# Kernel tuning notes

Hardware: AMD Instinct MI355X
Metric: run time of the kernel (lower is better)

Reference implementation:

```python
import jax, jax.numpy as jnp
import numpy as np

N = 100000   # nodes
E = 3200000  # edges (avg degree 32)
F = 10       # input features
H = 20       # hidden dim
G = 512      # graphs in batch
L = 2        # labels


def xavier(key, shape):
    fan_in, fan_out = shape[0], shape[1]
    a = jnp.sqrt(6.0 / (fan_in + fan_out))
    return jax.random.uniform(key, shape, jnp.float32, -a, a)


def setup_inputs() -> dict:
    key = jax.random.key(0)
    ks = jax.random.split(key, 12)
    x = jax.random.normal(ks[0], (N, F), jnp.float32)
    edge_index = jax.random.randint(ks[1], (2, E), 0, N, jnp.int64)
    batch = jnp.sort(jax.random.randint(ks[2], (N,), 0, G, jnp.int64))
    return {
        "x": x,
        "edge_index": edge_index,
        "batch": batch,
        # layer 1: F -> H
        "W_rel1": xavier(ks[3], (F, H)), "b1": jnp.zeros((H,), jnp.float32),
        "W_root1": xavier(ks[4], (F, H)),
        # layer 2: H -> H
        "W_rel2": xavier(ks[5], (H, H)), "b2": jnp.zeros((H,), jnp.float32),
        "W_root2": xavier(ks[6], (H, H)),
        # layer 3: H -> H
        "W_rel3": xavier(ks[7], (H, H)), "b3": jnp.zeros((H,), jnp.float32),
        "W_root3": xavier(ks[8], (H, H)),
        # readout linear: 2H -> L
        "W_lin": xavier(ks[9], (2 * H, L)), "b_lin": jnp.zeros((L,), jnp.float32),
    }


def _graph_conv(x, src, dst, W_rel, b, W_root):
    # PyG GraphConv: out = lin_rel(sum_{j->i} x_j) + lin_root(x_i)
    agg = jax.ops.segment_sum(x[src], dst, num_segments=N)  # [N, d_in]
    return agg @ W_rel + b + x @ W_root


def reference(x, edge_index, batch, W_rel1, b1, W_root1, W_rel2, b2, W_root2,
              W_rel3, b3, W_root3, W_lin, b_lin):
    src, dst = edge_index[0], edge_index[1]
    h = jax.nn.relu(_graph_conv(x, src, dst, W_rel1, b1, W_root1))
    h = jax.nn.relu(_graph_conv(h, src, dst, W_rel2, b2, W_root2))
    h = jax.nn.relu(_graph_conv(h, src, dst, W_rel3, b3, W_root3))  # [N, H]
    # global max / mean pool over graphs
    maxp = jax.ops.segment_max(h, batch, num_segments=G)            # [G, H]
    sump = jax.ops.segment_sum(h, batch, num_segments=G)            # [G, H]
    counts = jax.ops.segment_sum(jnp.ones((h.shape[0], 1), h.dtype), batch,
                                 num_segments=G)                    # [G, 1]
    nonempty = counts > 0
    maxp = jnp.where(nonempty, maxp, 0.0)
    meanp = sump / jnp.maximum(counts, 1.0)
    pooled = jnp.concatenate([maxp, meanp], axis=-1)                # [G, 2H]
    return pooled @ W_lin + b_lin
```

## Files before the change

### kernel.cpp

```cpp
#include <hip/hip_runtime.h>
#include <hip/hip_bf16.h>

#define NN 100000
#define FF 10
#define HH 20
#define GG 512
#define LL 2

#define NB 500
#define BNODES 200
#define CAP 7168
#define HB 100
#define SCAP 3712
#define TILE 4096
#define SRC_BITS 17
#define SRC_MASK 0x1FFFFu

__device__ inline unsigned short f2bf(float f) {
  unsigned u = __float_as_uint(f);
  unsigned r = u + 0x7FFFu + ((u >> 16) & 1u);
  return (unsigned short)(r >> 16);
}
__device__ inline float bflo(unsigned u) { return __uint_as_float(u << 16); }
__device__ inline float bfhi(unsigned u) { return __uint_as_float(u & 0xFFFF0000u); }

__global__ __launch_bounds__(256) void cast_init_kernel(
    const float* __restrict__ x, unsigned short* __restrict__ xb,
    float* __restrict__ sump, int* __restrict__ maxp, float* __restrict__ cnt,
    int* __restrict__ cursor, int n) {
  int i = blockIdx.x * 256 + threadIdx.x;
  if (i < n) xb[i] = f2bf(__builtin_nontemporal_load(x + i));
  if (i < GG * HH) {
    sump[i] = 0.0f;
    maxp[i] = 0;
  }
  if (i < GG) cnt[i] = 0.0f;
  if (i < NB) cursor[i] = 0;
}

__global__ __launch_bounds__(512) void multisplit_kernel(
    const int* __restrict__ src, const int* __restrict__ dst,
    int* __restrict__ cursor, unsigned int* __restrict__ pay, int E) {
  __shared__ int lhist[NB];
  __shared__ int lofs[NB];
  __shared__ int gbase[NB];
  __shared__ int lcur[NB];
  __shared__ unsigned int sord[TILE];
  __shared__ unsigned short sdbk[TILE];
  __shared__ int ss[512];
  int t = threadIdx.x;
  if (t < NB) lhist[t] = 0;
  __syncthreads();

  int base = blockIdx.x * TILE;
  int count = E - base;
  if (count > TILE) count = TILE;

  for (int i = t; i < count; i += 512)
    atomicAdd(&lhist[dst[base + i] / BNODES], 1);
  __syncthreads();

  int own = (t < NB) ? lhist[t] : 0;
  ss[t] = own;
  __syncthreads();
  for (int off = 1; off < 512; off <<= 1) {
    int a0 = (t >= off) ? ss[t - off] : 0;
    __syncthreads();
    ss[t] += a0;
    __syncthreads();
  }
  if (t < NB) {
    lofs[t] = ss[t] - own;
    int bo = own ? atomicAdd(&cursor[t], own) : 0;
    if (bo > CAP - own) bo = CAP - own;
    gbase[t] = t * CAP + bo;
    lcur[t] = 0;
  }
  __syncthreads();

  for (int i = t; i < count; i += 512) {
    int e = base + i;
    int d = __builtin_nontemporal_load(dst + e);
    int s = __builtin_nontemporal_load(src + e);
    int bk = d / BNODES;
    int ld = d - bk * BNODES;
    int r = atomicAdd(&lcur[bk], 1);
    int slot = lofs[bk] + r;
    sord[slot] = ((unsigned)ld << SRC_BITS) | (unsigned)s;
    sdbk[slot] = (unsigned short)bk;
  }
  __syncthreads();

  for (int i = t; i < count; i += 512) {
    int bk = sdbk[i];
    pay[gbase[bk] + (i - lofs[bk])] = sord[i];
  }
}

__global__ __launch_bounds__(256) void bucket_csr_kernel(
    const unsigned int* __restrict__ pay, const int* __restrict__ cursor,
    int* __restrict__ srt, int* __restrict__ rofs, int* __restrict__ rend) {
  __shared__ int lhist[BNODES];
  __shared__ int lofs[BNODES];
  __shared__ int lcur[BNODES];
  __shared__ int ss[256];
  int b = blockIdx.x;
  int t = threadIdx.x;
  int k0 = b * CAP;
  int ecnt = cursor[b];
  if (ecnt > CAP) ecnt = CAP;

  if (t < BNODES) lhist[t] = 0;
  __syncthreads();
  for (int k = t; k < ecnt; k += 256)
    atomicAdd(&lhist[pay[k0 + k] >> SRC_BITS], 1);
  __syncthreads();

  int own = (t < BNODES) ? lhist[t] : 0;
  ss[t] = own;
  __syncthreads();
  for (int off = 1; off < 256; off <<= 1) {
    int a0 = (t >= off) ? ss[t - off] : 0;
    __syncthreads();
    ss[t] += a0;
    __syncthreads();
  }
  if (t < BNODES) {
    int ex = ss[t] - own;
    lofs[t] = ex;
    lcur[t] = 0;
    rofs[b * BNODES + t] = k0 + ex;
    rend[b * BNODES + t] = k0 + ex + own;
  }
  __syncthreads();

  for (int k = t; k < ecnt; k += 256) {
    unsigned p = pay[k0 + k];
    int ld = p >> SRC_BITS;
    int r = atomicAdd(&lcur[ld], 1);
    srt[k0 + lofs[ld] + r] = (int)(p & SRC_MASK);
  }
}

template<int DIN>
__global__ __launch_bounds__(512) void bucket_layer_kernel(
    const unsigned short* __restrict__ hin, const int* __restrict__ srt,
    const int* __restrict__ rofs, const int* __restrict__ rend,
    const float* __restrict__ Wrel, const float* __restrict__ bias,
    const float* __restrict__ Wroot, unsigned short* __restrict__ hout) {
  constexpr int AST = (DIN == 10) ? 11 : 21;
  constexpr int CH = DIN / 5;
  __shared__ int sSrc[SCAP];
  __shared__ float acc[HB * AST];
  __shared__ unsigned short roots[HB * DIN];
  __shared__ float sWrel[DIN * HH];
  __shared__ float sWroot[DIN * HH];
  __shared__ float sb[HH];
  __shared__ int sRofs[HB];
  __shared__ int sRend[HB];
  __shared__ int sSeg0, sSegLen;
  int b2 = blockIdx.x;
  int t = threadIdx.x;
  int nbase = b2 * HB;

  for (int i = t; i < DIN * HH; i += 512) {
    sWrel[i] = Wrel[i];
    sWroot[i] = Wroot[i];
  }
  if (t < HH) sb[t] = bias[t];
  if (t < HB) {
    sRofs[t] = rofs[nbase + t];
    sRend[t] = rend[nbase + t];
  }
  if (t == 0) {
    int s0 = rofs[nbase];
    int sl = rend[nbase + HB - 1] - s0;
    sSeg0 = s0;
    sSegLen = sl < SCAP ? sl : SCAP;
  }
  {
    const unsigned* rs = (const unsigned*)(hin + (size_t)nbase * DIN);
    unsigned* rd = (unsigned*)roots;
    for (int i = t; i < HB * DIN / 2; i += 512) rd[i] = rs[i];
  }
  __syncthreads();

  int seg0 = sSeg0, seglen = sSegLen;
  for (int i = t; i < seglen; i += 512) sSrc[i] = srt[seg0 + i];
  __syncthreads();

  if (t < HB * 5) {
    int ln = t / 5;
    int c = t - ln * 5;
    int k0 = sRofs[ln] - seg0;
    int k1 = sRend[ln] - seg0;
    if (k1 > seglen) k1 = seglen;
    float a0 = 0, a1 = 0, a2 = 0, a3 = 0;
    const unsigned short* xb = hin + c * CH;
    if (CH == 4) {
      for (int k = k0; k < k1; k++) {
        uint2 u = *(const uint2*)(xb + (size_t)sSrc[k] * DIN);
        a0 += bflo(u.x);
        a1 += bfhi(u.x);
        a2 += bflo(u.y);
        a3 += bfhi(u.y);
      }
    } else {
      for (int k = k0; k < k1; k++) {
        unsigned u = *(const unsigned*)(xb + (size_t)sSrc[k] * DIN);
        a0 += bflo(u);
        a1 += bfhi(u);
      }
    }
    float* a = acc + ln * AST + c * CH;
    if (CH == 4) {
      a[0] = a0; a[1] = a1; a[2] = a2; a[3] = a3;
    } else {
      a[0] = a0; a[1] = a1;
    }
  }
  __syncthreads();

  for (int idx = t; idx < HB * HH; idx += 512) {
    int ln = idx / HH;
    int j = idx - ln * HH;
    const float* a = acc + ln * AST;
    const unsigned short* r = roots + ln * DIN;
    float v = sb[j];
#pragma unroll
    for (int f = 0; f < DIN; f++) {
      v += a[f] * sWrel[f * HH + j];
      v += bflo((unsigned)r[f]) * sWroot[f * HH + j];
    }
    hout[(size_t)nbase * HH + idx] = f2bf(fmaxf(v, 0.0f));
  }
}

__global__ __launch_bounds__(512) void bucket_layer_pool_kernel(
    const unsigned short* __restrict__ hin, const int* __restrict__ srt,
    const int* __restrict__ rofs, const int* __restrict__ rend,
    const float* __restrict__ Wrel, const float* __restrict__ bias,
    const float* __restrict__ Wroot, const int* __restrict__ batch,
    float* __restrict__ sump, int* __restrict__ maxp,
    float* __restrict__ cnt) {
  constexpr int DIN = 20;
  constexpr int AST = 21;
  __shared__ int sSrc[SCAP];
  __shared__ float acc[HB * AST];
  __shared__ unsigned short roots[HB * DIN];
  __shared__ int sBatch[HB];
  __shared__ float sWrel[DIN * HH];
  __shared__ float sWroot[DIN * HH];
  __shared__ float sb[HH];
  __shared__ int sRofs[HB];
  __shared__ int sRend[HB];
  __shared__ int sSeg0, sSegLen;
  int b2 = blockIdx.x;
  int t = threadIdx.x;
  int nbase = b2 * HB;

  for (int i = t; i < DIN * HH; i += 512) {
    sWrel[i] = Wrel[i];
    sWroot[i] = Wroot[i];
  }
  if (t < HH) sb[t] = bias[t];
  if (t < HB) {
    sRofs[t] = rofs[nbase + t];
    sRend[t] = rend[nbase + t];
    sBatch[t] = batch[nbase + t];
  }
  if (t == 0) {
    int s0 = rofs[nbase];
    int sl = rend[nbase + HB - 1] - s0;
    sSeg0 = s0;
    sSegLen = sl < SCAP ? sl : SCAP;
  }
  {
    const unsigned* rs = (const unsigned*)(hin + (size_t)nbase * DIN);
    unsigned* rd = (unsigned*)roots;
    for (int i = t; i < HB * DIN / 2; i += 512) rd[i] = rs[i];
  }
  __syncthreads();

  int seg0 = sSeg0, seglen = sSegLen;
  for (int i = t; i < seglen; i += 512) sSrc[i] = srt[seg0 + i];
  __syncthreads();

  if (t < HB * 5) {
    int ln = t / 5;
    int c = t - ln * 5;
    int k0 = sRofs[ln] - seg0;
    int k1 = sRend[ln] - seg0;
    if (k1 > seglen) k1 = seglen;
    float a0 = 0, a1 = 0, a2 = 0, a3 = 0;
    const unsigned short* xb = hin + c * 4;
    for (int k = k0; k < k1; k++) {
      uint2 u = *(const uint2*)(xb + (size_t)sSrc[k] * 20);
      a0 += bflo(u.x);
      a1 += bfhi(u.x);
      a2 += bflo(u.y);
      a3 += bfhi(u.y);
    }
    float* a = acc + ln * AST + c * 4;
    a[0] = a0; a[1] = a1; a[2] = a2; a[3] = a3;
  }
  __syncthreads();

  float vreg[4];
#pragma unroll
  for (int u = 0; u < 4; u++) {
    int idx = t + u * 512;
    if (idx < HB * HH) {
      int ln = idx / HH;
      int j = idx - ln * HH;
      const float* a = acc + ln * AST;
      const unsigned short* r = roots + ln * DIN;
      float v = sb[j];
#pragma unroll
      for (int f = 0; f < DIN; f++) {
        v += a[f] * sWrel[f * HH + j];
        v += bflo((unsigned)r[f]) * sWroot[f * HH + j];
      }
      vreg[u] = fmaxf(v, 0.0f);
    }
  }
  __syncthreads();
#pragma unroll
  for (int u = 0; u < 4; u++) {
    int idx = t + u * 512;
    if (idx < HB * HH) {
      int ln = idx / HH;
      int j = idx - ln * HH;
      acc[ln * AST + j] = vreg[u];
    }
  }
  __syncthreads();

  int g0 = sBatch[0];
  int g1 = sBatch[HB - 1];
  int ngr = g1 - g0 + 1;
  for (int it = t; it < ngr * HH; it += 512) {
    int gi = it / HH;
    int j = it - gi * HH;
    int g = g0 + gi;
    float s = 0.0f, m = 0.0f;
    int c = 0;
    for (int ln = 0; ln < HB; ln++) {
      if (sBatch[ln] == g) {
        float v = acc[ln * AST + j];
        s += v;
        m = fmaxf(m, v);
        c++;
      }
    }
    if (c) {
      atomicAdd(&sump[g * HH + j], s);
      atomicMax(&maxp[g * HH + j], __float_as_int(m));
      if (j == 0) atomicAdd(&cnt[g], (float)c);
    }
  }
}

__global__ __launch_bounds__(256) void readout_kernel(
    const float* __restrict__ sump, const int* __restrict__ maxp,
    const float* __restrict__ cnt, const float* __restrict__ Wlin,
    const float* __restrict__ blin, float* __restrict__ out) {
  int idx = blockIdx.x * 256 + threadIdx.x;
  if (idx >= GG * LL) return;
  int g = idx / LL;
  int l = idx - g * LL;
  float c = cnt[g];
  float inv = 1.0f / fmaxf(c, 1.0f);
  float acc = blin[l];
#pragma unroll
  for (int j = 0; j < HH; j++) {
    float mx = __int_as_float(maxp[g * HH + j]);
    float mean = sump[g * HH + j] * inv;
    acc += mx * Wlin[j * LL + l];
    acc += mean * Wlin[(HH + j) * LL + l];
  }
  out[idx] = acc;
}

extern "C" void kernel_launch(void* const* d_in, const int* in_sizes, int n_in,
                              void* d_out, int out_size, void* d_ws,
                              size_t ws_size, hipStream_t stream) {
  const float* x = (const float*)d_in[0];
  const int* edge_index = (const int*)d_in[1];
  const int* batch = (const int*)d_in[2];
  const float* W_rel1 = (const float*)d_in[3];
  const float* b1 = (const float*)d_in[4];
  const float* W_root1 = (const float*)d_in[5];
  const float* W_rel2 = (const float*)d_in[6];
  const float* b2 = (const float*)d_in[7];
  const float* W_root2 = (const float*)d_in[8];
  const float* W_rel3 = (const float*)d_in[9];
  const float* b3 = (const float*)d_in[10];
  const float* W_root3 = (const float*)d_in[11];
  const float* W_lin = (const float*)d_in[12];
  const float* b_lin = (const float*)d_in[13];
  float* out = (float*)d_out;

  const int E = in_sizes[1] / 2;
  const int n_nodes = in_sizes[0] / FF;
  const int* src = edge_index;
  const int* dst = edge_index + E;

  unsigned int* pay = (unsigned int*)d_ws;
  int* srt = (int*)(pay + (size_t)NB * CAP);
  int* rofs = srt + (size_t)NB * CAP;
  int* rend = rofs + NN;
  int* cursor = rend + NN;
  float* sump = (float*)(cursor + 512);
  int* maxp = (int*)(sump + GG * HH);
  float* cnt = (float*)(maxp + GG * HH);
  unsigned short* xb = (unsigned short*)(cnt + 512);
  unsigned short* h1 = xb + (size_t)NN * FF;
  unsigned short* h2 = h1 + (size_t)NN * HH;

  const int edge_tiles = (E + TILE - 1) / TILE;

  cast_init_kernel<<<(n_nodes * FF + 255) / 256, 256, 0, stream>>>(
      x, xb, sump, maxp, cnt, cursor, n_nodes * FF);

  multisplit_kernel<<<edge_tiles, 512, 0, stream>>>(src, dst, cursor, pay, E);
  bucket_csr_kernel<<<NB, 256, 0, stream>>>(pay, cursor, srt, rofs, rend);

  bucket_layer_kernel<FF><<<NB * 2, 512, 0, stream>>>(
      xb, srt, rofs, rend, W_rel1, b1, W_root1, h1);
  bucket_layer_kernel<HH><<<NB * 2, 512, 0, stream>>>(
      h1, srt, rofs, rend, W_rel2, b2, W_root2, h2);
  bucket_layer_pool_kernel<<<NB * 2, 512, 0, stream>>>(
      h2, srt, rofs, rend, W_rel3, b3, W_root3, batch, sump, maxp, cnt);

  readout_kernel<<<(GG * LL + 255) / 256, 256, 0, stream>>>(
      sump, maxp, cnt, W_lin, b_lin, out);
}
```

Baseline: 259.1 us.

## Pad bf16 feature rows to 16/24 and balance edge gathers across threads

Feature buffers are stored padded (16 bf16 for input, 24 for hidden) so every gather can fetch 8 features with one 16-byte load. Edge work in each node block is now split into equal-length contiguous ranges per thread group, with a binary search to find the starting node and shared-memory atomics to combine partial sums at node boundaries. The previous scheme gave one thread per node and so suffered load imbalance. The dense transform is also vectorised with float4 weight reads and fp32 roots. The cost is extra bytes per gathered row for the padding and shared atomics where ranges cross nodes.

```diff
diff --git a/kernel.cpp b/kernel.cpp
--- a/kernel.cpp
+++ b/kernel.cpp
@@ -15,6 +15,8 @@
 #define TILE 4096
 #define SRC_BITS 17
 #define SRC_MASK 0x1FFFFu
+#define XPAD 16
+#define HPAD 24
 
 __device__ inline unsigned short f2bf(float f) {
   unsigned u = __float_as_uint(f);
@@ -27,9 +29,15 @@
 __global__ __launch_bounds__(256) void cast_init_kernel(
     const float* __restrict__ x, unsigned short* __restrict__ xb,
     float* __restrict__ sump, int* __restrict__ maxp, float* __restrict__ cnt,
-    int* __restrict__ cursor, int n) {
+    int* __restrict__ cursor, int n16) {
   int i = blockIdx.x * 256 + threadIdx.x;
-  if (i < n) xb[i] = f2bf(__builtin_nontemporal_load(x + i));
+  if (i < n16) {
+    int node = i >> 4;
+    int f = i & 15;
+    float v = 0.0f;
+    if (f < FF) v = __builtin_nontemporal_load(x + (size_t)node * FF + f);
+    xb[i] = f2bf(v);
+  }
   if (i < GG * HH) {
     sump[i] = 0.0f;
     maxp[i] = 0;
@@ -142,19 +150,20 @@
   }
 }
 
-template<int DIN>
-__global__ __launch_bounds__(512) void bucket_layer_kernel(
+template<int DL, int DSI, int DSO>
+__global__ __launch_bounds__(512) void layer_kernel(
     const unsigned short* __restrict__ hin, const int* __restrict__ srt,
     const int* __restrict__ rofs, const int* __restrict__ rend,
     const float* __restrict__ Wrel, const float* __restrict__ bias,
     const float* __restrict__ Wroot, unsigned short* __restrict__ hout) {
-  constexpr int AST = (DIN == 10) ? 11 : 21;
-  constexpr int CH = DIN / 5;
+  constexpr int CL = DSI / 8;
+  constexpr int NG = 512 / CL;
+  constexpr int AST = DSI + 1;
   __shared__ int sSrc[SCAP];
   __shared__ float acc[HB * AST];
-  __shared__ unsigned short roots[HB * DIN];
-  __shared__ float sWrel[DIN * HH];
-  __shared__ float sWroot[DIN * HH];
+  __shared__ float rootsf[HB * DL];
+  __shared__ __align__(16) float sWrel[DL * HH];
+  __shared__ __align__(16) float sWroot[DL * HH];
   __shared__ float sb[HH];
   __shared__ int sRofs[HB];
   __shared__ int sRend[HB];
@@ -163,7 +172,7 @@
   int t = threadIdx.x;
   int nbase = b2 * HB;
 
-  for (int i = t; i < DIN * HH; i += 512) {
+  for (int i = t; i < DL * HH; i += 512) {
     sWrel[i] = Wrel[i];
     sWroot[i] = Wroot[i];
   }
@@ -178,88 +187,116 @@
     sSeg0 = s0;
     sSegLen = sl < SCAP ? sl : SCAP;
   }
-  {
-    const unsigned* rs = (const unsigned*)(hin + (size_t)nbase * DIN);
-    unsigned* rd = (unsigned*)roots;
-    for (int i = t; i < HB * DIN / 2; i += 512) rd[i] = rs[i];
-  }
+  for (int i = t; i < HB * (DL / 2); i += 512) {
+    int ln = i / (DL / 2);
+    int p = i - ln * (DL / 2);
+    unsigned u = *(const unsigned*)(hin + (size_t)(nbase + ln) * DSI + 2 * p);
+    rootsf[ln * DL + 2 * p] = bflo(u);
+    rootsf[ln * DL + 2 * p + 1] = bfhi(u);
+  }
+  for (int i = t; i < HB * AST; i += 512) acc[i] = 0.0f;
   __syncthreads();
 
   int seg0 = sSeg0, seglen = sSegLen;
-  for (int i = t; i < seglen; i += 512) sSrc[i] = srt[seg0 + i];
+  for (int i = t; i < seglen; i += 512)
+    sSrc[i] = __builtin_nontemporal_load(srt + seg0 + i);
+  __syncthreads();
+
+  int g = t / CL;
+  int c = t - g * CL;
+  if (g < NG) {
+    int W = (seglen + NG - 1) / NG;
+    int a = g * W;
+    if (a > seglen) a = seglen;
+    int b = a + W;
+    if (b > seglen) b = seglen;
+    if (a < b) {
+      int lo = 0, hi = HB - 1;
+      while (lo < hi) {
+        int mid = (lo + hi + 1) >> 1;
+        if (sRofs[mid] - seg0 <= a) lo = mid; else hi = mid - 1;
+      }
+      int ln = lo;
+      const unsigned short* basep = hin + c * 8;
+      float a0 = 0, a1 = 0, a2 = 0, a3 = 0, a4 = 0, a5 = 0, a6 = 0, a7 = 0;
+      int k = a;
+      while (k < b) {
+        int lim = sRend[ln] - seg0;
+        if (lim > b) lim = b;
+#pragma clang loop unroll_count(4)
+        for (; k < lim; ++k) {
+          int s = sSrc[k];
+          uint4 u = *(const uint4*)(basep + (size_t)s * DSI);
+          a0 += bflo(u.x); a1 += bfhi(u.x);
+          a2 += bflo(u.y); a3 += bfhi(u.y);
+          a4 += bflo(u.z); a5 += bfhi(u.z);
+          a6 += bflo(u.w); a7 += bfhi(u.w);
+        }
+        float* ap = acc + ln * AST + c * 8;
+        atomicAdd(ap + 0, a0); atomicAdd(ap + 1, a1);
+        atomicAdd(ap + 2, a2); atomicAdd(ap + 3, a3);
+        atomicAdd(ap + 4, a4); atomicAdd(ap + 5, a5);
+        atomicAdd(ap + 6, a6); atomicAdd(ap + 7, a7);
+        a0 = a1 = a2 = a3 = a4 = a5 = a6 = a7 = 0.0f;
+        ln++;
+      }
+    }
+  }
   __syncthreads();
 
   if (t < HB * 5) {
     int ln = t / 5;
-    int c = t - ln * 5;
-    int k0 = sRofs[ln] - seg0;
-    int k1 = sRend[ln] - seg0;
-    if (k1 > seglen) k1 = seglen;
-    float a0 = 0, a1 = 0, a2 = 0, a3 = 0;
-    const unsigned short* xb = hin + c * CH;
-    if (CH == 4) {
-      for (int k = k0; k < k1; k++) {
-        uint2 u = *(const uint2*)(xb + (size_t)sSrc[k] * DIN);
-        a0 += bflo(u.x);
-        a1 += bfhi(u.x);
-        a2 += bflo(u.y);
-        a3 += bfhi(u.y);
-      }
-    } else {
-      for (int k = k0; k < k1; k++) {
-        unsigned u = *(const unsigned*)(xb + (size_t)sSrc[k] * DIN);
-        a0 += bflo(u);
-        a1 += bfhi(u);
-      }
+    int jg = t - ln * 5;
+    int j0 = jg * 4;
+    float v0 = sb[j0], v1 = sb[j0 + 1], v2 = sb[j0 + 2], v3 = sb[j0 + 3];
+    const float* ap = acc + ln * AST;
+    const float* rp = rootsf + ln * DL;
+#pragma unroll
+    for (int f = 0; f < DL; ++f) {
+      float af = ap[f], rf = rp[f];
+      float4 wr = *(const float4*)(sWrel + f * HH + j0);
+      float4 wo = *(const float4*)(sWroot + f * HH + j0);
+      v0 += af * wr.x + rf * wo.x;
+      v1 += af * wr.y + rf * wo.y;
+      v2 += af * wr.z + rf * wo.z;
+      v3 += af * wr.w + rf * wo.w;
     }
-    float* a = acc + ln * AST + c * CH;
-    if (CH == 4) {
-      a[0] = a0; a[1] = a1; a[2] = a2; a[3] = a3;
-    } else {
-      a[0] = a0; a[1] = a1;
-    }
-  }
-  __syncthreads();
-
-  for (int idx = t; idx < HB * HH; idx += 512) {
-    int ln = idx / HH;
-    int j = idx - ln * HH;
-    const float* a = acc + ln * AST;
-    const unsigned short* r = roots + ln * DIN;
-    float v = sb[j];
+    unsigned short* orow = hout + (size_t)(nbase + ln) * DSO;
+    uint2 o;
+    o.x = ((unsigned)f2bf(fmaxf(v1, 0.0f)) << 16) | f2bf(fmaxf(v0, 0.0f));
+    o.y = ((unsigned)f2bf(fmaxf(v3, 0.0f)) << 16) | f2bf(fmaxf(v2, 0.0f));
+    *(uint2*)(orow + j0) = o;
+  }
+  if (t < HB) {
+    unsigned short* orow = hout + (size_t)(nbase + t) * DSO;
 #pragma unroll
-    for (int f = 0; f < DIN; f++) {
-      v += a[f] * sWrel[f * HH + j];
-      v += bflo((unsigned)r[f]) * sWroot[f * HH + j];
-    }
-    hout[(size_t)nbase * HH + idx] = f2bf(fmaxf(v, 0.0f));
-  }
-}
-
-__global__ __launch_bounds__(512) void bucket_layer_pool_kernel(
+    for (int e = HH; e < DSO; ++e) orow[e] = 0;
+  }
+}
+
+__global__ __launch_bounds__(512) void layer_pool_kernel(
     const unsigned short* __restrict__ hin, const int* __restrict__ srt,
     const int* __restrict__ rofs, const int* __restrict__ rend,
     const float* __restrict__ Wrel, const float* __restrict__ bias,
     const float* __restrict__ Wroot, const int* __restrict__ batch,
     float* __restrict__ sump, int* __restrict__ maxp,
     float* __restrict__ cnt) {
-  constexpr int DIN = 20;
-  constexpr int AST = 21;
+  constexpr int DL = 20, DSI = 24, CL = 3, NG = 170, AST = 25;
   __shared__ int sSrc[SCAP];
   __shared__ float acc[HB * AST];
-  __shared__ unsigned short roots[HB * DIN];
-  __shared__ int sBatch[HB];
-  __shared__ float sWrel[DIN * HH];
-  __shared__ float sWroot[DIN * HH];
+  __shared__ float rootsf[HB * DL];
+  __shared__ __align__(16) float sWrel[DL * HH];
+  __shared__ __align__(16) float sWroot[DL * HH];
   __shared__ float sb[HH];
   __shared__ int sRofs[HB];
   __shared__ int sRend[HB];
+  __shared__ int sBatch[HB];
   __shared__ int sSeg0, sSegLen;
   int b2 = blockIdx.x;
   int t = threadIdx.x;
   int nbase = b2 * HB;
 
-  for (int i = t; i < DIN * HH; i += 512) {
+  for (int i = t; i < DL * HH; i += 512) {
     sWrel[i] = Wrel[i];
     sWroot[i] = Wroot[i];
   }
@@ -275,64 +312,89 @@
     sSeg0 = s0;
     sSegLen = sl < SCAP ? sl : SCAP;
   }
-  {
-    const unsigned* rs = (const unsigned*)(hin + (size_t)nbase * DIN);
-    unsigned* rd = (unsigned*)roots;
-    for (int i = t; i < HB * DIN / 2; i += 512) rd[i] = rs[i];
-  }
+  for (int i = t; i < HB * (DL / 2); i += 512) {
+    int ln = i / (DL / 2);
+    int p = i - ln * (DL / 2);
+    unsigned u = *(const unsigned*)(hin + (size_t)(nbase + ln) * DSI + 2 * p);
+    rootsf[ln * DL + 2 * p] = bflo(u);
+    rootsf[ln * DL + 2 * p + 1] = bfhi(u);
+  }
+  for (int i = t; i < HB * AST; i += 512) acc[i] = 0.0f;
   __syncthreads();
 
   int seg0 = sSeg0, seglen = sSegLen;
-  for (int i = t; i < seglen; i += 512) sSrc[i] = srt[seg0 + i];
-  __syncthreads();
-
+  for (int i = t; i < seglen; i += 512)
+    sSrc[i] = __builtin_nontemporal_load(srt + seg0 + i);
+  __syncthreads();
+
+  int g = t / CL;
+  int c = t - g * CL;
+  if (g < NG) {
+    int W = (seglen + NG - 1) / NG;
+    int a = g * W;
+    if (a > seglen) a = seglen;
+    int b = a + W;
+    if (b > seglen) b = seglen;
+    if (a < b) {
+      int lo = 0, hi = HB - 1;
+      while (lo < hi) {
+        int mid = (lo + hi + 1) >> 1;
+        if (sRofs[mid] - seg0 <= a) lo = mid; else hi = mid - 1;
+      }
+      int ln = lo;
+      const unsigned short* basep = hin + c * 8;
+      float a0 = 0, a1 = 0, a2 = 0, a3 = 0, a4 = 0, a5 = 0, a6 = 0, a7 = 0;
+      int k = a;
+      while (k < b) {
+        int lim = sRend[ln] - seg0;
+        if (lim > b) lim = b;
+#pragma clang loop unroll_count(4)
+        for (; k < lim; ++k) {
+          int s = sSrc[k];
+          uint4 u = *(const uint4*)(basep + (size_t)s * DSI);
+          a0 += bflo(u.x); a1 += bfhi(u.x);
+          a2 += bflo(u.y); a3 += bfhi(u.y);
+          a4 += bflo(u.z); a5 += bfhi(u.z);
+          a6 += bflo(u.w); a7 += bfhi(u.w);
+        }
+        float* ap = acc + ln * AST + c * 8;
+        atomicAdd(ap + 0, a0); atomicAdd(ap + 1, a1);
+        atomicAdd(ap + 2, a2); atomicAdd(ap + 3, a3);
+        atomicAdd(ap + 4, a4); atomicAdd(ap + 5, a5);
+        atomicAdd(ap + 6, a6); atomicAdd(ap + 7, a7);
+        a0 = a1 = a2 = a3 = a4 = a5 = a6 = a7 = 0.0f;
+        ln++;
+      }
+    }
+  }
+  __syncthreads();
+
+  float v0 = 0, v1 = 0, v2 = 0, v3 = 0;
+  int ln0 = 0, j0 = 0;
   if (t < HB * 5) {
-    int ln = t / 5;
-    int c = t - ln * 5;
-    int k0 = sRofs[ln] - seg0;
-    int k1 = sRend[ln] - seg0;
-    if (k1 > seglen) k1 = seglen;
-    float a0 = 0, a1 = 0, a2 = 0, a3 = 0;
-    const unsigned short* xb = hin + c * 4;
-    for (int k = k0; k < k1; k++) {
-      uint2 u = *(const uint2*)(xb + (size_t)sSrc[k] * 20);
-      a0 += bflo(u.x);
-      a1 += bfhi(u.x);
-      a2 += bflo(u.y);
-      a3 += bfhi(u.y);
+    ln0 = t / 5;
+    int jg = t - ln0 * 5;
+    j0 = jg * 4;
+    v0 = sb[j0]; v1 = sb[j0 + 1]; v2 = sb[j0 + 2]; v3 = sb[j0 + 3];
+    const float* ap = acc + ln0 * AST;
+    const float* rp = rootsf + ln0 * DL;
+#pragma unroll
+    for (int f = 0; f < DL; ++f) {
+      float af = ap[f], rf = rp[f];
+      float4 wr = *(const float4*)(sWrel + f * HH + j0);
+      float4 wo = *(const float4*)(sWroot + f * HH + j0);
+      v0 += af * wr.x + rf * wo.x;
+      v1 += af * wr.y + rf * wo.y;
+      v2 += af * wr.z + rf * wo.z;
+      v3 += af * wr.w + rf * wo.w;
     }
-    float* a = acc + ln * AST + c * 4;
-    a[0] = a0; a[1] = a1; a[2] = a2; a[3] = a3;
-  }
-  __syncthreads();
-
-  float vreg[4];
-#pragma unroll
-  for (int u = 0; u < 4; u++) {
-    int idx = t + u * 512;
-    if (idx < HB * HH) {
-      int ln = idx / HH;
-      int j = idx - ln * HH;
-      const float* a = acc + ln * AST;
-      const unsigned short* r = roots + ln * DIN;
-      float v = sb[j];
-#pragma unroll
-      for (int f = 0; f < DIN; f++) {
-        v += a[f] * sWrel[f * HH + j];
-        v += bflo((unsigned)r[f]) * sWroot[f * HH + j];
-      }
-      vreg[u] = fmaxf(v, 0.0f);
-    }
-  }
-  __syncthreads();
-#pragma unroll
-  for (int u = 0; u < 4; u++) {
-    int idx = t + u * 512;
-    if (idx < HB * HH) {
-      int ln = idx / HH;
-      int j = idx - ln * HH;
-      acc[ln * AST + j] = vreg[u];
-    }
+    v0 = fmaxf(v0, 0.0f); v1 = fmaxf(v1, 0.0f);
+    v2 = fmaxf(v2, 0.0f); v3 = fmaxf(v3, 0.0f);
+  }
+  __syncthreads();
+  if (t < HB * 5) {
+    float* ap = acc + ln0 * AST + j0;
+    ap[0] = v0; ap[1] = v1; ap[2] = v2; ap[3] = v3;
   }
   __syncthreads();
 
@@ -342,21 +404,21 @@
   for (int it = t; it < ngr * HH; it += 512) {
     int gi = it / HH;
     int j = it - gi * HH;
-    int g = g0 + gi;
+    int gph = g0 + gi;
     float s = 0.0f, m = 0.0f;
-    int c = 0;
+    int c2 = 0;
     for (int ln = 0; ln < HB; ln++) {
-      if (sBatch[ln] == g) {
+      if (sBatch[ln] == gph) {
         float v = acc[ln * AST + j];
         s += v;
         m = fmaxf(m, v);
-        c++;
+        c2++;
       }
     }
-    if (c) {
-      atomicAdd(&sump[g * HH + j], s);
-      atomicMax(&maxp[g * HH + j], __float_as_int(m));
-      if (j == 0) atomicAdd(&cnt[g], (float)c);
+    if (c2) {
+      atomicAdd(&sump[gph * HH + j], s);
+      atomicMax(&maxp[gph * HH + j], __float_as_int(m));
+      if (j == 0) atomicAdd(&cnt[gph], (float)c2);
     }
   }
 }
@@ -415,22 +477,22 @@
   int* maxp = (int*)(sump + GG * HH);
   float* cnt = (float*)(maxp + GG * HH);
   unsigned short* xb = (unsigned short*)(cnt + 512);
-  unsigned short* h1 = xb + (size_t)NN * FF;
-  unsigned short* h2 = h1 + (size_t)NN * HH;
+  unsigned short* h1 = xb + (size_t)NN * XPAD;
+  unsigned short* h2 = h1 + (size_t)NN * HPAD;
 
   const int edge_tiles = (E + TILE - 1) / TILE;
 
-  cast_init_kernel<<<(n_nodes * FF + 255) / 256, 256, 0, stream>>>(
-      x, xb, sump, maxp, cnt, cursor, n_nodes * FF);
+  cast_init_kernel<<<(n_nodes * XPAD + 255) / 256, 256, 0, stream>>>(
+      x, xb, sump, maxp, cnt, cursor, n_nodes * XPAD);
 
   multisplit_kernel<<<edge_tiles, 512, 0, stream>>>(src, dst, cursor, pay, E);
   bucket_csr_kernel<<<NB, 256, 0, stream>>>(pay, cursor, srt, rofs, rend);
 
-  bucket_layer_kernel<FF><<<NB * 2, 512, 0, stream>>>(
+  layer_kernel<FF, XPAD, HPAD><<<NB * 2, 512, 0, stream>>>(
       xb, srt, rofs, rend, W_rel1, b1, W_root1, h1);
-  bucket_layer_kernel<HH><<<NB * 2, 512, 0, stream>>>(
+  layer_kernel<HH, HPAD, HPAD><<<NB * 2, 512, 0, stream>>>(
       h1, srt, rofs, rend, W_rel2, b2, W_root2, h2);
-  bucket_layer_pool_kernel<<<NB * 2, 512, 0, stream>>>(
+  layer_pool_kernel<<<NB * 2, 512, 0, stream>>>(
       h2, srt, rofs, rend, W_rel3, b3, W_root3, batch, sump, maxp, cnt);
 
   readout_kernel<<<(GG * LL + 255) / 256, 256, 0, stream>>>(
```

Result: slower. 313.4 us (+21.0%).
